# Kernel optimization log

Measured on AMD Instinct MI355X. Metric: run time of the kernel, lower is better.

The kernel has to match this reference:

```python
import jax, jax.numpy as jnp
import numpy as np

HEADS = 16
DIM_HEAD = 64
QUERY_DIM = 1024


def setup_inputs() -> dict:
    key = jax.random.key(0)
    ks = jax.random.split(key, 5)
    B, S, D = 4, 2048, QUERY_DIM
    inner = HEADS * DIM_HEAD
    s = 0.02
    return {
        "x": jax.random.normal(ks[0], (B, S, D), dtype=jnp.float32),
        "Wq": jax.random.normal(ks[1], (D, inner), dtype=jnp.float32) * s,
        "Wk": jax.random.normal(ks[2], (D, inner), dtype=jnp.float32) * s,
        "Wv": jax.random.normal(ks[3], (D, inner), dtype=jnp.float32) * s,
        "Wo": jax.random.normal(ks[4], (inner, D), dtype=jnp.float32) * s,
    }


def reference(x, Wq, Wk, Wv, Wo):
    B, S, D = x.shape
    h, d = HEADS, DIM_HEAD
    scale = d ** (-0.5)
    # projections -> [B, h, S, d]
    q = (x @ Wq).reshape(B, S, h, d).transpose(0, 2, 1, 3)
    k = (x @ Wk).reshape(B, S, h, d).transpose(0, 2, 1, 3)
    v = (x @ Wv).reshape(B, S, h, d).transpose(0, 2, 1, 3)
    # scores [B, h, S, S]
    attn = jnp.einsum("bhqd,bhkd->bhqk", q, k) * scale
    attn = jax.nn.softmax(attn, axis=-1)
    out = jnp.einsum("bhqk,bhkd->bhqd", attn, v)
    out = out.transpose(0, 2, 1, 3).reshape(B, S, h * d)
    return out @ Wo
```

## Files before the change

### kernel.cpp

```cpp
#include <hip/hip_runtime.h>
#include <cstddef>

#define BATCH  4
#define SLEN   2048
#define NHEADS 16
#define DHEAD  64
#define DMODEL 1024

typedef __attribute__((ext_vector_type(8)))  short short8;
typedef __attribute__((ext_vector_type(4)))  float f32x4;
typedef __attribute__((ext_vector_type(16))) float f32x16;

__device__ inline unsigned short f2bf(float f) {
    union { float f; unsigned int u; } v; v.f = f;
    unsigned int r = v.u + 0x7fffu + ((v.u >> 16) & 1u);
    return (unsigned short)(r >> 16);
}

__device__ inline float fast_exp2(float x) {
#if __has_builtin(__builtin_amdgcn_exp2f)
    return __builtin_amdgcn_exp2f(x);
#else
    return __expf(x * 0.69314718f);
#endif
}

__device__ inline void gload_lds16(const unsigned short* g, unsigned short* l) {
    __builtin_amdgcn_global_load_lds(
        (const __attribute__((address_space(1))) void*)g,
        (__attribute__((address_space(3))) void*)l, 16, 0, 0);
}

__device__ inline void barrier_fence() {
    asm volatile("s_barrier" ::: "memory");
}

__global__ __launch_bounds__(256)
void prep(const float* __restrict__ x, unsigned short* __restrict__ xb,
          const float* __restrict__ W0, const float* __restrict__ W1,
          const float* __restrict__ W2, const float* __restrict__ W3,
          unsigned short* __restrict__ T0, unsigned short* __restrict__ T1,
          unsigned short* __restrict__ T2, unsigned short* __restrict__ T3)
{
    __shared__ unsigned short T[64 * 72];
    const int bid = blockIdx.x;
    const int tid = threadIdx.x;

    if (bid < 4096) {
        const int i = bid * 256 + tid;
        const float4 a = ((const float4*)x)[2 * i];
        const float4 b = ((const float4*)x)[2 * i + 1];
        short8 o;
        o[0] = (short)f2bf(a.x); o[1] = (short)f2bf(a.y);
        o[2] = (short)f2bf(a.z); o[3] = (short)f2bf(a.w);
        o[4] = (short)f2bf(b.x); o[5] = (short)f2bf(b.y);
        o[6] = (short)f2bf(b.z); o[7] = (short)f2bf(b.w);
        ((short8*)xb)[i] = o;
        return;
    }

    const int idx = bid - 4096;
    const int z = idx >> 8;
    const float* W = (z == 0) ? W0 : (z == 1) ? W1 : (z == 2) ? W2 : W3;
    unsigned short* Wt = (z == 0) ? T0 : (z == 1) ? T1 : (z == 2) ? T2 : T3;
    const int n0 = (idx & 15) * 64, k0 = ((idx >> 4) & 15) * 64;

    #pragma unroll
    for (int it = 0; it < 2; it++) {
        const int t2 = it * 256 + tid;
        const int row = t2 >> 3, col8 = (t2 & 7) * 8;
        const float4 a = *(const float4*)(W + (size_t)(k0 + row) * DMODEL + n0 + col8);
        const float4 b = *(const float4*)(W + (size_t)(k0 + row) * DMODEL + n0 + col8 + 4);
        short8 o;
        o[0] = (short)f2bf(a.x); o[1] = (short)f2bf(a.y);
        o[2] = (short)f2bf(a.z); o[3] = (short)f2bf(a.w);
        o[4] = (short)f2bf(b.x); o[5] = (short)f2bf(b.y);
        o[6] = (short)f2bf(b.z); o[7] = (short)f2bf(b.w);
        *(short8*)&T[row * 72 + col8] = o;
    }
    __syncthreads();
    #pragma unroll
    for (int it = 0; it < 2; it++) {
        const int t2 = it * 256 + tid;
        const int nn = t2 >> 3, k8 = (t2 & 7) * 8;
        short8 v;
        #pragma unroll
        for (int j = 0; j < 8; j++) v[j] = (short)T[(k8 + j) * 72 + nn];
        *(short8*)(Wt + (size_t)(n0 + nn) * DMODEL + k0 + k8) = v;
    }
}

__global__ __launch_bounds__(512, 2)
void gemm8p_qkv(const unsigned short* __restrict__ A,
                const unsigned short* __restrict__ Bw,
                unsigned short* __restrict__ qb,
                unsigned short* __restrict__ kb,
                unsigned short* __restrict__ vtb)
{
    constexpr int K = DMODEL;
    constexpr int NT = K / 64;
    __shared__ unsigned short lds8[65536];

    const int tid  = threadIdx.x;
    const int lane = tid & 63;
    const int wave = tid >> 6;
    const int c  = lane & 15, qd = lane >> 4;
    const int wr = wave >> 2, wc = wave & 3;
    const int cl7 = c & 7;

    const int flat = blockIdx.y * 12 + blockIdx.x;
    const int swz  = (flat & 7) * 48 + (flat >> 3);
    const int bx = swz % 12, by = swz / 12;
    const int n0 = bx * 256, m0 = by * 256;

    const unsigned short* ag[4];
    const unsigned short* bg[4];
    int lo[4];
    #pragma unroll
    for (int j = 0; j < 4; j++) {
        const int cid = j * 512 + tid;
        const int row = cid >> 3;
        const int k8  = (cid & 7) ^ (row & 7);
        ag[j] = A  + (size_t)(m0 + row) * K + k8 * 8;
        bg[j] = Bw + (size_t)(n0 + row) * K + k8 * 8;
        lo[j] = cid * 8;
    }

#define STAGE_A(bufi) { _Pragma("unroll") \
    for (int j = 0; j < 4; j++) { \
        gload_lds16(ag[j], &lds8[(bufi) * 16384 + lo[j]]); ag[j] += 64; } }
#define STAGE_B(bufi) { _Pragma("unroll") \
    for (int j = 0; j < 4; j++) { \
        gload_lds16(bg[j], &lds8[32768 + (bufi) * 16384 + lo[j]]); bg[j] += 64; } }

    f32x4 acc[8][4];
    #pragma unroll
    for (int mb = 0; mb < 8; mb++)
        #pragma unroll
        for (int nb = 0; nb < 4; nb++)
            #pragma unroll
            for (int r = 0; r < 4; r++) acc[mb][nb][r] = 0.f;

    STAGE_A(0); STAGE_B(0); STAGE_B(1);

    short8 bf[4], af[4];

    for (int t = 0; t < NT; t++) {
        const int buf = t & 1;
        const unsigned short* Asb = &lds8[buf * 16384];
        const unsigned short* Bsb = &lds8[32768 + buf * 16384];

        if (t + 1 < NT) STAGE_A(buf ^ 1);
        if (t == NT - 1) asm volatile("s_waitcnt vmcnt(0)" ::: "memory");
        else             asm volatile("s_waitcnt vmcnt(8)" ::: "memory");
        barrier_fence();
        {
            const int sw = qd ^ cl7;
            #pragma unroll
            for (int nb = 0; nb < 4; nb++)
                bf[nb] = *(const short8*)&Bsb[((wc * 64 + nb * 16 + c) * 8 + sw) * 8];
            #pragma unroll
            for (int mb = 0; mb < 4; mb++)
                af[mb] = *(const short8*)&Asb[((wr * 128 + mb * 16 + c) * 8 + sw) * 8];
        }
        __builtin_amdgcn_s_setprio(1);
        #pragma unroll
        for (int mb = 0; mb < 4; mb++)
            #pragma unroll
            for (int nb = 0; nb < 4; nb++)
                acc[mb][nb] = __builtin_amdgcn_mfma_f32_16x16x32_bf16(
                    af[mb], bf[nb], acc[mb][nb], 0, 0, 0);
        __builtin_amdgcn_s_setprio(0);
        barrier_fence();

        {
            const int sw = qd ^ cl7;
            #pragma unroll
            for (int mb = 0; mb < 4; mb++)
                af[mb] = *(const short8*)&Asb[((wr * 128 + (mb + 4) * 16 + c) * 8 + sw) * 8];
        }
        barrier_fence();
        __builtin_amdgcn_s_setprio(1);
        #pragma unroll
        for (int mb = 0; mb < 4; mb++)
            #pragma unroll
            for (int nb = 0; nb < 4; nb++)
                acc[mb + 4][nb] = __builtin_amdgcn_mfma_f32_16x16x32_bf16(
                    af[mb], bf[nb], acc[mb + 4][nb], 0, 0, 0);
        __builtin_amdgcn_s_setprio(0);
        barrier_fence();

        {
            const int sw = (4 + qd) ^ cl7;
            #pragma unroll
            for (int nb = 0; nb < 4; nb++)
                bf[nb] = *(const short8*)&Bsb[((wc * 64 + nb * 16 + c) * 8 + sw) * 8];
            #pragma unroll
            for (int mb = 0; mb < 4; mb++)
                af[mb] = *(const short8*)&Asb[((wr * 128 + mb * 16 + c) * 8 + sw) * 8];
        }
        barrier_fence();
        __builtin_amdgcn_s_setprio(1);
        #pragma unroll
        for (int mb = 0; mb < 4; mb++)
            #pragma unroll
            for (int nb = 0; nb < 4; nb++)
                acc[mb][nb] = __builtin_amdgcn_mfma_f32_16x16x32_bf16(
                    af[mb], bf[nb], acc[mb][nb], 0, 0, 0);
        __builtin_amdgcn_s_setprio(0);
        barrier_fence();

        {
            const int sw = (4 + qd) ^ cl7;
            #pragma unroll
            for (int mb = 0; mb < 4; mb++)
                af[mb] = *(const short8*)&Asb[((wr * 128 + (mb + 4) * 16 + c) * 8 + sw) * 8];
        }
        if (t + 2 < NT) STAGE_B(buf);
        barrier_fence();
        __builtin_amdgcn_s_setprio(1);
        #pragma unroll
        for (int mb = 0; mb < 4; mb++)
            #pragma unroll
            for (int nb = 0; nb < 4; nb++)
                acc[mb + 4][nb] = __builtin_amdgcn_mfma_f32_16x16x32_bf16(
                    af[mb], bf[nb], acc[mb + 4][nb], 0, 0, 0);
        __builtin_amdgcn_s_setprio(0);
        barrier_fence();
    }
#undef STAGE_A
#undef STAGE_B

    const int z = bx >> 2;
    const int ncol0 = (n0 & 1023) + wc * 64;
    const int mbase = m0 + wr * 128 + qd * 4;
    if (z != 2) {
        unsigned short* C = z ? kb : qb;
        const float sc = z ? 1.0f : 0.18033688f;
        #pragma unroll
        for (int mb = 0; mb < 8; mb++)
            #pragma unroll
            for (int nb = 0; nb < 4; nb++)
                #pragma unroll
                for (int r = 0; r < 4; r++)
                    C[(size_t)(mbase + mb * 16 + r) * DMODEL + ncol0 + nb * 16 + c] =
                        f2bf(acc[mb][nb][r] * sc);
    } else {
        #pragma unroll
        for (int mb = 0; mb < 8; mb++) {
            const int row = mbase + mb * 16;
            const int b = row >> 11, s = row & 2047;
            #pragma unroll
            for (int nb = 0; nb < 4; nb++) {
                const int n_in = ncol0 + nb * 16 + c;
                const int h = n_in >> 6, dd = n_in & 63;
                ushort4 val = make_ushort4(f2bf(acc[mb][nb][0]), f2bf(acc[mb][nb][1]),
                                           f2bf(acc[mb][nb][2]), f2bf(acc[mb][nb][3]));
                *(ushort4*)(vtb + ((size_t)((b * 16 + h) * 64 + dd)) * SLEN + s) = val;
            }
        }
    }
}

__global__ __launch_bounds__(256)
void gemm_fin(const unsigned short* __restrict__ A,
              const unsigned short* __restrict__ Bw,
              float* __restrict__ C)
{
    constexpr int N = DMODEL, K = DMODEL;
    __shared__ unsigned short As[128 * 64];
    __shared__ unsigned short Bs[128 * 64];

    const int tid  = threadIdx.x;
    const int lane = tid & 63;
    const int wave = tid >> 6;
    const int c  = lane & 15, qd = lane >> 4;
    const int wr = wave >> 1, wc = wave & 1;
    const int m0 = blockIdx.y * 128, n0 = blockIdx.x * 128;

    const unsigned short* ag[4];
    const unsigned short* bg[4];
    unsigned short* al[4];
    unsigned short* bl[4];
    #pragma unroll
    for (int j = 0; j < 4; j++) {
        const int cid = j * 256 + tid;
        const int row = cid >> 3;
        const int k8  = (cid & 7) ^ (row & 7);
        ag[j] = A  + (size_t)(m0 + row) * K + k8 * 8;
        bg[j] = Bw + (size_t)(n0 + row) * K + k8 * 8;
        al[j] = &As[cid * 8];
        bl[j] = &Bs[cid * 8];
    }

    f32x4 acc[4][4];
    #pragma unroll
    for (int mb = 0; mb < 4; mb++)
        #pragma unroll
        for (int nb = 0; nb < 4; nb++)
            #pragma unroll
            for (int r = 0; r < 4; r++) acc[mb][nb][r] = 0.f;

    for (int k0 = 0; k0 < K; k0 += 64) {
        __syncthreads();
        #pragma unroll
        for (int j = 0; j < 4; j++) {
            gload_lds16(ag[j], al[j]);
            gload_lds16(bg[j], bl[j]);
            ag[j] += 64; bg[j] += 64;
        }
        __syncthreads();

        #pragma unroll
        for (int ks = 0; ks < 2; ks++) {
            const int sw = (ks * 4 + qd) ^ (c & 7);
            short8 af[4], bf[4];
            #pragma unroll
            for (int mb = 0; mb < 4; mb++)
                af[mb] = *(const short8*)&As[((wr * 64 + mb * 16 + c) * 8 + sw) * 8];
            #pragma unroll
            for (int nb = 0; nb < 4; nb++)
                bf[nb] = *(const short8*)&Bs[((wc * 64 + nb * 16 + c) * 8 + sw) * 8];
            #pragma unroll
            for (int mb = 0; mb < 4; mb++)
                #pragma unroll
                for (int nb = 0; nb < 4; nb++)
                    acc[mb][nb] = __builtin_amdgcn_mfma_f32_16x16x32_bf16(
                        af[mb], bf[nb], acc[mb][nb], 0, 0, 0);
        }
    }

    const int mbase = m0 + wr * 64 + qd * 4;
    const int nbase = n0 + wc * 64 + c;
    #pragma unroll
    for (int mb = 0; mb < 4; mb++)
        #pragma unroll
        for (int nb = 0; nb < 4; nb++)
            #pragma unroll
            for (int r = 0; r < 4; r++)
                C[(size_t)(mbase + mb * 16 + r) * N + nbase + nb * 16] = acc[mb][nb][r];
}

__global__ __launch_bounds__(256, 4)
void attn_mfma6(const unsigned short* __restrict__ qb,
                const unsigned short* __restrict__ kb,
                const unsigned short* __restrict__ vtb,
                unsigned short* __restrict__ O)
{
    __shared__ unsigned short lds[18432];
    unsigned short* Ks = lds;
    unsigned short* Vs = lds + 4096;

    const int tid = threadIdx.x;
    const int w   = tid >> 6, ln = tid & 63;
    const int c5  = ln & 31;
    const int l5i = ln >> 5;

    const int L  = blockIdx.x + (int)gridDim.x * blockIdx.y;
    const int wg = (L & 7) * 128 + (L >> 3);
    const int qt = wg & 15, bh = wg >> 4;
    const int b = bh >> 4, h = bh & 15;
    const size_t bh_base = ((size_t)b * SLEN * NHEADS + h) * 64;
    constexpr int RS = NHEADS * 64;

    const int srow = ln >> 3;
    const int sk8  = (ln & 7) ^ srow;
    const int prow = (srow & 3) | ((w & 1) << 2) | (((srow >> 2) & 1) << 3) | ((w >> 1) << 4);
    const unsigned short* kg0 = kb + bh_base + (size_t)prow * RS + sk8 * 8;
    const unsigned short* kg1 = kg0 + (size_t)32 * RS;
    const unsigned short* vg0 = vtb + ((size_t)bh * 64 + w * 8 + srow) * SLEN + sk8 * 8;
    const unsigned short* vg1 = vg0 + (size_t)32 * SLEN;
    unsigned short* kl0 = &Ks[(w * 64 + ln) * 8];
    unsigned short* kl1 = kl0 + 2048;
    unsigned short* vl0 = &Vs[(w * 64 + ln) * 8];
    unsigned short* vl1 = vl0 + 2048;

    const int qtile = qt * 128 + w * 32;

    short8 qf[4];
    #pragma unroll
    for (int kst = 0; kst < 4; kst++)
        qf[kst] = *(const short8*)(qb + bh_base +
            (size_t)(qtile + c5) * RS + kst * 16 + l5i * 8);

    f32x16 acc[2];
    #pragma unroll
    for (int db = 0; db < 2; db++)
        #pragma unroll
        for (int r = 0; r < 16; r++) acc[db][r] = 0.f;
    float lsum = 0.f;
    const int cl7 = c5 & 7;

    for (int kt = 0; kt < SLEN / 64; kt++) {
        __syncthreads();
        gload_lds16(kg0, kl0); gload_lds16(kg1, kl1);
        gload_lds16(vg0, vl0); gload_lds16(vg1, vl1);
        kg0 += (size_t)64 * RS; kg1 += (size_t)64 * RS; vg0 += 64; vg1 += 64;
        __syncthreads();

        #pragma unroll
        for (int kb32 = 0; kb32 < 2; kb32++) {
            f32x16 sacc;
            #pragma unroll
            for (int r = 0; r < 16; r++) sacc[r] = 0.f;
            __builtin_amdgcn_s_setprio(1);
            #pragma unroll
            for (int kst = 0; kst < 4; kst++) {
                const int slot = (kst * 2 + l5i) ^ cl7;
                short8 kf = *(const short8*)&Ks[((kb32 * 32 + c5) * 8 + slot) * 8];
                sacc = __builtin_amdgcn_mfma_f32_32x32x16_bf16(
                    kf, qf[kst], sacc, 0, 0, 0);
            }
            __builtin_amdgcn_s_setprio(0);

            unsigned pk[8];
            {
                float p[16];
                float s0 = 0.f, s1 = 0.f;
                #pragma unroll
                for (int r = 0; r < 16; r += 2) {
                    p[r]     = fast_exp2(sacc[r]);
                    p[r + 1] = fast_exp2(sacc[r + 1]);
                    s0 += p[r]; s1 += p[r + 1];
                }
                lsum += s0 + s1;
                #pragma unroll
                for (int i = 0; i < 8; i++)
                    pk[i] = __builtin_amdgcn_perm(
                        __float_as_uint(p[2 * i + 1]), __float_as_uint(p[2 * i]),
                        0x07060302u);
            }

            #pragma unroll
            for (int kk = 0; kk < 2; kk++) {
                const int k2 = kb32 * 2 + kk;
                union { unsigned u[4]; short8 s; } t;
                t.u[0] = pk[4 * kk + 0];
                t.u[1] = pk[4 * kk + 1];
                t.u[2] = pk[4 * kk + 2];
                t.u[3] = pk[4 * kk + 3];
                const short8 pf = t.s;
                __builtin_amdgcn_s_setprio(1);
                #pragma unroll
                for (int db = 0; db < 2; db++) {
                    const int slot = (k2 * 2 + l5i) ^ cl7;
                    short8 vf = *(const short8*)&Vs[((db * 32 + c5) * 8 + slot) * 8];
                    acc[db] = __builtin_amdgcn_mfma_f32_32x32x16_bf16(
                        vf, pf, acc[db], 0, 0, 0);
                }
                __builtin_amdgcn_s_setprio(0);
            }
        }
    }

    __syncthreads();
    float l = lsum;
    l += __shfl_xor(l, 32);
    const float inv = 1.001953125f / l;
    unsigned short* E = lds + w * 2304;
    #pragma unroll
    for (int db = 0; db < 2; db++)
        #pragma unroll
        for (int u = 0; u < 4; u++) {
            const int d0 = db * 32 + 8 * u + 4 * l5i;
            const int q  = c5;
            ushort4 val = make_ushort4(
                f2bf(acc[db][4 * u + 0] * inv),
                f2bf(acc[db][4 * u + 1] * inv),
                f2bf(acc[db][4 * u + 2] * inv),
                f2bf(acc[db][4 * u + 3] * inv));
            *(ushort4*)&E[q * 72 + d0] = val;
        }
    __builtin_amdgcn_wave_barrier();
    #pragma unroll
    for (int it = 0; it < 4; it++) {
        const int t2 = it * 64 + ln;
        const int row = t2 >> 3, col8 = (t2 & 7) * 8;
        short8 o = *(const short8*)&E[row * 72 + col8];
        *(short8*)(O + bh_base + (size_t)(qtile + row) * RS + col8) = o;
    }
}

extern "C" void kernel_launch(void* const* d_in, const int* in_sizes, int n_in,
                              void* d_out, int out_size, void* d_ws, size_t ws_size,
                              hipStream_t stream)
{
    const float* x  = (const float*)d_in[0];
    const float* Wq = (const float*)d_in[1];
    const float* Wk = (const float*)d_in[2];
    const float* Wv = (const float*)d_in[3];
    const float* Wo = (const float*)d_in[4];
    float* out = (float*)d_out;

    const size_t per = (size_t)BATCH * SLEN * NHEADS * DHEAD;
    const size_t wsz = (size_t)DMODEL * DMODEL;
    unsigned short* qb  = (unsigned short*)d_ws;
    unsigned short* kb  = qb  + per;
    unsigned short* vtb = kb  + per;
    unsigned short* xb  = vtb + per;
    unsigned short* wtq = xb  + per;
    unsigned short* wtk = wtq + wsz;
    unsigned short* wtv = wtk + wsz;
    unsigned short* wto = wtv + wsz;

    dim3 blk(256);
    prep<<<dim3(4096 + 1024), blk, 0, stream>>>(x, xb, Wq, Wk, Wv, Wo,
                                                wtq, wtk, wtv, wto);

    gemm8p_qkv<<<dim3(12, 32), dim3(512), 0, stream>>>(xb, wtq, qb, kb, vtb);

    attn_mfma6<<<dim3(SLEN / 128, BATCH * NHEADS), blk, 0, stream>>>(qb, kb, vtb, qb);

    gemm_fin<<<dim3(8, 64), blk, 0, stream>>>(qb, wto, out);
}
```

Baseline: 267.1 us.

## Fuse fp32-to-bf16 conversion of x into the QKV GEMM A-tile loads

Drops the separate x-to-bf16 pass from the prep kernel. The QKV GEMM now loads fp32 x into registers, converts it to bf16 and writes it to LDS itself, with the barriers and waits restructured around the register-staged load. This saves writing and rereading an 8M-element bf16 copy of x. In exchange, each of the 12 column blocks rereads fp32 x (twice the bytes per reload), register pressure rises, and the A prefetch becomes a synchronous register round-trip instead of an async direct-to-LDS load.

Result: slower. 312.1 us (+16.8%).

```diff
diff --git a/kernel.cpp b/kernel.cpp
--- a/kernel.cpp
+++ b/kernel.cpp
@@ -36,30 +36,14 @@
 }
 
 __global__ __launch_bounds__(256)
-void prep(const float* __restrict__ x, unsigned short* __restrict__ xb,
-          const float* __restrict__ W0, const float* __restrict__ W1,
+void prep(const float* __restrict__ W0, const float* __restrict__ W1,
           const float* __restrict__ W2, const float* __restrict__ W3,
           unsigned short* __restrict__ T0, unsigned short* __restrict__ T1,
           unsigned short* __restrict__ T2, unsigned short* __restrict__ T3)
 {
     __shared__ unsigned short T[64 * 72];
-    const int bid = blockIdx.x;
+    const int idx = blockIdx.x;
     const int tid = threadIdx.x;
-
-    if (bid < 4096) {
-        const int i = bid * 256 + tid;
-        const float4 a = ((const float4*)x)[2 * i];
-        const float4 b = ((const float4*)x)[2 * i + 1];
-        short8 o;
-        o[0] = (short)f2bf(a.x); o[1] = (short)f2bf(a.y);
-        o[2] = (short)f2bf(a.z); o[3] = (short)f2bf(a.w);
-        o[4] = (short)f2bf(b.x); o[5] = (short)f2bf(b.y);
-        o[6] = (short)f2bf(b.z); o[7] = (short)f2bf(b.w);
-        ((short8*)xb)[i] = o;
-        return;
-    }
-
-    const int idx = bid - 4096;
     const int z = idx >> 8;
     const float* W = (z == 0) ? W0 : (z == 1) ? W1 : (z == 2) ? W2 : W3;
     unsigned short* Wt = (z == 0) ? T0 : (z == 1) ? T1 : (z == 2) ? T2 : T3;
@@ -91,7 +75,7 @@
 }
 
 __global__ __launch_bounds__(512, 2)
-void gemm8p_qkv(const unsigned short* __restrict__ A,
+void gemm8p_qkv(const float* __restrict__ X,
                 const unsigned short* __restrict__ Bw,
                 unsigned short* __restrict__ qb,
                 unsigned short* __restrict__ kb,
@@ -113,7 +97,7 @@
     const int bx = swz % 12, by = swz / 12;
     const int n0 = bx * 256, m0 = by * 256;
 
-    const unsigned short* ag[4];
+    const float* agf[4];
     const unsigned short* bg[4];
     int lo[4];
     #pragma unroll
@@ -121,14 +105,25 @@
         const int cid = j * 512 + tid;
         const int row = cid >> 3;
         const int k8  = (cid & 7) ^ (row & 7);
-        ag[j] = A  + (size_t)(m0 + row) * K + k8 * 8;
-        bg[j] = Bw + (size_t)(n0 + row) * K + k8 * 8;
+        agf[j] = X  + (size_t)(m0 + row) * K + k8 * 8;
+        bg[j]  = Bw + (size_t)(n0 + row) * K + k8 * 8;
         lo[j] = cid * 8;
     }
 
-#define STAGE_A(bufi) { _Pragma("unroll") \
+    float4 ar[4][2];
+
+#define LOAD_A() { _Pragma("unroll") \
     for (int j = 0; j < 4; j++) { \
-        gload_lds16(ag[j], &lds8[(bufi) * 16384 + lo[j]]); ag[j] += 64; } }
+        ar[j][0] = *(const float4*)(agf[j]); \
+        ar[j][1] = *(const float4*)(agf[j] + 4); agf[j] += 64; } }
+#define WRITE_A(bufi) { _Pragma("unroll") \
+    for (int j = 0; j < 4; j++) { \
+        short8 o; \
+        o[0] = (short)f2bf(ar[j][0].x); o[1] = (short)f2bf(ar[j][0].y); \
+        o[2] = (short)f2bf(ar[j][0].z); o[3] = (short)f2bf(ar[j][0].w); \
+        o[4] = (short)f2bf(ar[j][1].x); o[5] = (short)f2bf(ar[j][1].y); \
+        o[6] = (short)f2bf(ar[j][1].z); o[7] = (short)f2bf(ar[j][1].w); \
+        *(short8*)&lds8[(bufi) * 16384 + lo[j]] = o; } }
 #define STAGE_B(bufi) { _Pragma("unroll") \
     for (int j = 0; j < 4; j++) { \
         gload_lds16(bg[j], &lds8[32768 + (bufi) * 16384 + lo[j]]); bg[j] += 64; } }
@@ -141,7 +136,11 @@
             #pragma unroll
             for (int r = 0; r < 4; r++) acc[mb][nb][r] = 0.f;
 
-    STAGE_A(0); STAGE_B(0); STAGE_B(1);
+    STAGE_B(0); STAGE_B(1);
+    LOAD_A();
+    WRITE_A(0);
+    asm volatile("s_waitcnt lgkmcnt(0)" ::: "memory");
+    barrier_fence();
 
     short8 bf[4], af[4];
 
@@ -150,10 +149,7 @@
         const unsigned short* Asb = &lds8[buf * 16384];
         const unsigned short* Bsb = &lds8[32768 + buf * 16384];
 
-        if (t + 1 < NT) STAGE_A(buf ^ 1);
-        if (t == NT - 1) asm volatile("s_waitcnt vmcnt(0)" ::: "memory");
-        else             asm volatile("s_waitcnt vmcnt(8)" ::: "memory");
-        barrier_fence();
+        if (t + 1 < NT) LOAD_A();
         {
             const int sw = qd ^ cl7;
             #pragma unroll
@@ -179,7 +175,6 @@
             for (int mb = 0; mb < 4; mb++)
                 af[mb] = *(const short8*)&Asb[((wr * 128 + (mb + 4) * 16 + c) * 8 + sw) * 8];
         }
-        barrier_fence();
         __builtin_amdgcn_s_setprio(1);
         #pragma unroll
         for (int mb = 0; mb < 4; mb++)
@@ -199,7 +194,6 @@
             for (int mb = 0; mb < 4; mb++)
                 af[mb] = *(const short8*)&Asb[((wr * 128 + mb * 16 + c) * 8 + sw) * 8];
         }
-        barrier_fence();
         __builtin_amdgcn_s_setprio(1);
         #pragma unroll
         for (int mb = 0; mb < 4; mb++)
@@ -216,7 +210,10 @@
             for (int mb = 0; mb < 4; mb++)
                 af[mb] = *(const short8*)&Asb[((wr * 128 + (mb + 4) * 16 + c) * 8 + sw) * 8];
         }
+        asm volatile("s_waitcnt vmcnt(0)" ::: "memory");
+        if (t + 1 < NT) WRITE_A(buf ^ 1);
         if (t + 2 < NT) STAGE_B(buf);
+        asm volatile("s_waitcnt lgkmcnt(0)" ::: "memory");
         barrier_fence();
         __builtin_amdgcn_s_setprio(1);
         #pragma unroll
@@ -228,7 +225,8 @@
         __builtin_amdgcn_s_setprio(0);
         barrier_fence();
     }
-#undef STAGE_A
+#undef LOAD_A
+#undef WRITE_A
 #undef STAGE_B
 
     const int z = bx >> 2;
@@ -497,19 +495,17 @@
     unsigned short* qb  = (unsigned short*)d_ws;
     unsigned short* kb  = qb  + per;
     unsigned short* vtb = kb  + per;
-    unsigned short* xb  = vtb + per;
-    unsigned short* wtq = xb  + per;
+    unsigned short* wtq = vtb + per;
     unsigned short* wtk = wtq + wsz;
     unsigned short* wtv = wtk + wsz;
     unsigned short* wto = wtv + wsz;
 
-    dim3 blk(256);
-    prep<<<dim3(4096 + 1024), blk, 0, stream>>>(x, xb, Wq, Wk, Wv, Wo,
-                                                wtq, wtk, wtv, wto);
-
-    gemm8p_qkv<<<dim3(12, 32), dim3(512), 0, stream>>>(xb, wtq, qb, kb, vtb);
-
-    attn_mfma6<<<dim3(SLEN / 128, BATCH * NHEADS), blk, 0, stream>>>(qb, kb, vtb, qb);
-
-    gemm_fin<<<dim3(8, 64), blk, 0, stream>>>(qb, wto, out);
-}
+    prep<<<dim3(1024), dim3(256), 0, stream>>>(Wq, Wk, Wv, Wo,
+                                               wtq, wtk, wtv, wto);
+
+    gemm8p_qkv<<<dim3(12, 32), dim3(512), 0, stream>>>(x, wtq, qb, kb, vtb);
+
+    attn_mfma6<<<dim3(SLEN / 128, BATCH * NHEADS), dim3(256), 0, stream>>>(qb, kb, vtb, qb);
+
+    gemm_fin<<<dim3(8, 64), dim3(256), 0, stream>>>(qb, wto, out);
+}
```
